# Kernel tuning notes

Measured on AMD Instinct MI355X. Metric: run time of the kernel, lower is better.

The kernel has to match this reference:

```python
import jax, jax.numpy as jnp
import numpy as np

DIM = 192
HEADS = 6
WS = 8                      # window size (Wh = Ww = 8)
N = WS * WS                 # tokens per window = 64
NW = 1024                   # windows per image (256/8)^2
BATCH = 2
B_ = NW * BATCH             # 2048 windows total
TABLE = (2 * WS - 1) ** 2   # 225 relative-position entries


def _relative_position_index():
    coords = np.stack(np.meshgrid(np.arange(WS), np.arange(WS), indexing='ij'))  # (2,WS,WS)
    cf = coords.reshape(2, -1)                       # (2, N)
    rc = (cf[:, :, None] - cf[:, None, :]).transpose(1, 2, 0).astype(np.int64)  # (N,N,2)
    rc[..., 0] += WS - 1
    rc[..., 1] += WS - 1
    rc[..., 0] *= 2 * WS - 1
    return rc.sum(-1)                                # (N, N) in [0, TABLE)


def setup_inputs() -> dict:
    key = jax.random.key(0)
    ks = jax.random.split(key, 16)
    s = 0.02
    inp = {
        'x': jax.random.normal(ks[0], (B_, N, DIM), jnp.float32),
        'y': jax.random.normal(ks[1], (B_, N, DIM), jnp.float32),
        'mask_x': jnp.zeros((NW, N, N), jnp.float32),
        'mask_y': jnp.zeros((NW, N, N), jnp.float32),
        'qkv_w': jax.random.normal(ks[2], (3 * DIM, DIM), jnp.float32) * s,
        'qkv_b': jnp.zeros((3 * DIM,), jnp.float32),
        'kv_w': jax.random.normal(ks[3], (2 * DIM, DIM), jnp.float32) * s,
        'kv_b': jnp.zeros((2 * DIM,), jnp.float32),
        'rpb_x': jax.random.normal(ks[4], (TABLE, HEADS), jnp.float32) * s,
        'rpb_y': jax.random.normal(ks[5], (TABLE, HEADS), jnp.float32) * s,
        'merge1_w': jax.random.normal(ks[6], (DIM, 2 * DIM), jnp.float32) * s,
        'merge1_b': jnp.zeros((DIM,), jnp.float32),
        'merge2_w': jax.random.normal(ks[7], (DIM, DIM), jnp.float32) * s,
        'merge2_b': jnp.zeros((DIM,), jnp.float32),
        'proj_w': jax.random.normal(ks[8], (DIM, DIM), jnp.float32) * s,
        'proj_b': jnp.zeros((DIM,), jnp.float32),
        'rel_idx': jnp.asarray(_relative_position_index(), jnp.int32),
    }
    return inp


def _attend(q, k, v, table, rel_idx, mask):
    # q,k,v: (B_, H, N, hd); table: (TABLE, H); mask: (nW, N, N)
    b_, h, n, hd = q.shape
    bias = table[rel_idx].transpose(2, 0, 1)                 # (H, N, N)
    attn = jnp.einsum('bhnd,bhmd->bhnm', q, k) + bias[None]  # (B_, H, N, N)
    nW = mask.shape[0]
    attn = attn.reshape(b_ // nW, nW, h, n, n) + mask[None, :, None]
    attn = jax.nn.softmax(attn.reshape(b_, h, n, n), axis=-1)
    out = jnp.einsum('bhnm,bhmd->bhnd', attn, v)             # (B_, H, N, hd)
    return out.transpose(0, 2, 1, 3).reshape(b_, n, h * hd)


def reference(x, y, mask_x, mask_y, qkv_w, qkv_b, kv_w, kv_b, rpb_x, rpb_y,
              merge1_w, merge1_b, merge2_w, merge2_b, proj_w, proj_b, rel_idx):
    b_, n, c = x.shape
    hd = c // HEADS
    scale = hd ** (-0.5)
    qkv = (x @ qkv_w.T + qkv_b).reshape(b_, n, 3, HEADS, hd).transpose(2, 0, 3, 1, 4)
    q, k, v = qkv[0] * scale, qkv[1], qkv[2]
    x_self = _attend(q, k, v, rpb_x, rel_idx, mask_x)
    kv = (y @ kv_w.T + kv_b).reshape(b_, n, 2, HEADS, hd).transpose(2, 0, 3, 1, 4)
    x_cross = _attend(q, kv[0], kv[1], rpb_y, rel_idx, mask_y)
    m = jnp.concatenate([x_self, x_cross], axis=-1) @ merge1_w.T + merge1_b
    m = jax.nn.leaky_relu(m, negative_slope=0.2)
    m = m @ merge2_w.T + merge2_b
    return m @ proj_w.T + proj_b
```

## Files before the change

### kernel.cpp

```cpp
#include <hip/hip_runtime.h>

#define DEVINL __device__ __forceinline__

typedef __attribute__((ext_vector_type(8))) short          s16x8;
typedef __attribute__((ext_vector_type(8))) unsigned short u16x8;
typedef __attribute__((ext_vector_type(4))) unsigned short u16x4;
typedef __attribute__((ext_vector_type(4))) float          f32x4;

DEVINL unsigned short f2b(float f) {
    union { float f; unsigned int u; } c; c.f = f;
    return (unsigned short)((c.u + 0x7FFFu + ((c.u >> 16) & 1u)) >> 16);
}
DEVINL f32x4 mfma16(s16x8 a, s16x8 b, f32x4 c) {
    return __builtin_amdgcn_mfma_f32_16x16x32_bf16(a, b, c, 0, 0, 0);
}

#define QKV_ELEMS 110592
#define KV_ELEMS  73728
#define M1_ELEMS  73728
#define M2_ELEMS  36864
#define PW_ELEMS  36864
#define O_QKV 0
#define O_KV  110592
#define O_M1  184320
#define O_M2  258048
#define O_PW  294912
#define WB_ELEMS 331776
#define WB_BYTES (WB_ELEMS * 2)

#define LD_IN  200
#define LD_K   200
#define LD_VT  72
#define LD_P   72
#define LD_CAT 392
#define LD_M   200
#define OFF_R1 0
#define OFF_R2 12800
#define OFF_R3 25600
#define SMEM_ELEMS 39424
#define CATB OFF_R2

#define SCALE 0.17677669529663687f
#define LOG2E 1.4426950408889634f

__global__ __launch_bounds__(256) void cvt_w(
    const float* __restrict__ a, const float* __restrict__ b, const float* __restrict__ c,
    const float* __restrict__ d, const float* __restrict__ e, unsigned short* __restrict__ o)
{
    int i = (blockIdx.x * 256 + threadIdx.x) * 4;
    if (i >= WB_ELEMS) return;
    const float* s; int off;
    if (i < O_KV)      { s = a; off = i - O_QKV; }
    else if (i < O_M1) { s = b; off = i - O_KV; }
    else if (i < O_M2) { s = c; off = i - O_M1; }
    else if (i < O_PW) { s = d; off = i - O_M2; }
    else               { s = e; off = i - O_PW; }
    float4 v = *(const float4*)(s + off);
    u16x4 r;
    r[0] = f2b(v.x); r[1] = f2b(v.y); r[2] = f2b(v.z); r[3] = f2b(v.w);
    *(u16x4*)(o + i) = r;
}

template<bool WB>
DEVINL s16x8 loadB(const unsigned short* wbp, const float* wfp, int off) {
    if constexpr (WB) {
        return *(const s16x8*)(wbp + off);
    } else {
        float4 v0 = *(const float4*)(wfp + off);
        float4 v1 = *(const float4*)(wfp + off + 4);
        s16x8 r;
        r[0] = (short)f2b(v0.x); r[1] = (short)f2b(v0.y); r[2] = (short)f2b(v0.z); r[3] = (short)f2b(v0.w);
        r[4] = (short)f2b(v1.x); r[5] = (short)f2b(v1.y); r[6] = (short)f2b(v1.z); r[7] = (short)f2b(v1.w);
        return r;
    }
}

template<bool WB>
__global__ __launch_bounds__(512, 2) void swin_fused(
    const float* __restrict__ x,
    const float* __restrict__ y,
    const float* __restrict__ mask_x,
    const float* __restrict__ mask_y,
    const float* __restrict__ qkv_w,
    const float* __restrict__ qkv_b,
    const float* __restrict__ kv_w,
    const float* __restrict__ kv_b,
    const float* __restrict__ rpb_x,
    const float* __restrict__ rpb_y,
    const float* __restrict__ m1w,
    const float* __restrict__ m1b,
    const float* __restrict__ m2w,
    const float* __restrict__ m2b,
    const float* __restrict__ pw,
    const float* __restrict__ pb,
    const int* __restrict__ rel_idx,
    const unsigned short* __restrict__ wb,
    float* __restrict__ out)
{
    __shared__ __align__(16) unsigned short smem[SMEM_ELEMS];

    const int tid  = threadIdx.x;
    const int w    = tid >> 6;
    const int lane = tid & 63;
    const int l16  = lane & 15;
    const int quad = lane >> 4;
    const int wm   = w >> 2;
    const int wn   = w & 3;
    const int rb   = w >> 1;
    const int hh   = w & 1;
    const int b    = blockIdx.x;
    const int widx = b & 1023;

    const unsigned short* wqkv = WB ? wb + O_QKV : nullptr;
    const unsigned short* wkv  = WB ? wb + O_KV  : nullptr;
    const unsigned short* wm1  = WB ? wb + O_M1  : nullptr;
    const unsigned short* wm2  = WB ? wb + O_M2  : nullptr;
    const unsigned short* wpw  = WB ? wb + O_PW  : nullptr;

    {
        const float4* gx = (const float4*)(x + (size_t)b * 64 * 192);
        #pragma unroll
        for (int it = 0; it < 3; ++it) {
            int c = it * 512 + tid;
            int e = c * 8;
            int row = e / 192, col = e - row * 192;
            float4 v0 = gx[c * 2], v1 = gx[c * 2 + 1];
            u16x8 r;
            r[0] = f2b(v0.x); r[1] = f2b(v0.y); r[2] = f2b(v0.z); r[3] = f2b(v0.w);
            r[4] = f2b(v1.x); r[5] = f2b(v1.y); r[6] = f2b(v1.z); r[7] = f2b(v1.w);
            *(u16x8*)&smem[OFF_R1 + row * LD_IN + col] = r;
        }
    }
    __syncthreads();

    {
        s16x8 afr[2][6];
        #pragma unroll
        for (int mt = 0; mt < 2; ++mt)
            #pragma unroll
            for (int ks = 0; ks < 6; ++ks)
                afr[mt][ks] = *(const s16x8*)&smem[OFF_R1 + (wm * 32 + mt * 16 + l16) * LD_IN + ks * 32 + quad * 8];
        __syncthreads();

        #pragma unroll
        for (int nt = 0; nt < 9; ++nt) {
            int n0  = wn * 144 + nt * 16;
            int col = n0 + l16;
            f32x4 acc0 = {0,0,0,0}, acc1 = {0,0,0,0};
            #pragma unroll
            for (int ks = 0; ks < 6; ++ks) {
                s16x8 bf = loadB<WB>(wqkv, qkv_w, col * 192 + ks * 32 + quad * 8);
                acc0 = mfma16(afr[0][ks], bf, acc0);
                acc1 = mfma16(afr[1][ks], bf, acc1);
            }
            f32x4 accv[2] = {acc0, acc1};
            float bias = qkv_b[col];
            if (n0 < 192) {
                #pragma unroll
                for (int mt = 0; mt < 2; ++mt)
                    #pragma unroll
                    for (int r = 0; r < 4; ++r)
                        smem[OFF_R1 + (wm * 32 + mt * 16 + quad * 4 + r) * LD_K + col] =
                            f2b((accv[mt][r] + bias) * SCALE);
            } else if (n0 < 384) {
                #pragma unroll
                for (int mt = 0; mt < 2; ++mt)
                    #pragma unroll
                    for (int r = 0; r < 4; ++r)
                        smem[OFF_R2 + (wm * 32 + mt * 16 + quad * 4 + r) * LD_K + (col - 192)] =
                            f2b(accv[mt][r] + bias);
            } else {
                #pragma unroll
                for (int mt = 0; mt < 2; ++mt)
                    #pragma unroll
                    for (int r = 0; r < 4; ++r)
                        smem[OFF_R3 + (col - 384) * LD_VT + (wm * 32 + mt * 16 + quad * 4 + r)] =
                            f2b(accv[mt][r] + bias);
            }
        }
    }
    __syncthreads();

    s16x8 aQ[3];
    #pragma unroll
    for (int hl = 0; hl < 3; ++hl)
        aQ[hl] = *(const s16x8*)&smem[OFF_R1 + (rb * 16 + l16) * LD_K + (hh * 3 + hl) * 32 + quad * 8];
    __syncthreads();

    auto do_attn = [&](const float* __restrict__ rpb,
                       const float* __restrict__ mask,
                       unsigned (&opk)[12]) {
        f32x4 oacc[3][2];
        #pragma unroll
        for (int hl = 0; hl < 3; ++hl) { f32x4 z = {0,0,0,0}; oacc[hl][0] = z; oacc[hl][1] = z; }
        int   idxv[16];
        float maskv[16];
        #pragma unroll
        for (int i = 0; i < 16; ++i) {
            int ntt = i >> 2, r = i & 3;
            int row = rb * 16 + quad * 4 + r;
            int col = ntt * 16 + l16;
            idxv[i]  = rel_idx[row * 64 + col];
            maskv[i] = mask[(size_t)widx * 4096 + row * 64 + col];
        }
        const int pbase = OFF_R1 + w * 16 * LD_P;
        #pragma unroll
        for (int hl = 0; hl < 3; ++hl) {
            int h = hh * 3 + hl;
            f32x4 sacc[4];
            #pragma unroll
            for (int ntt = 0; ntt < 4; ++ntt) {
                s16x8 bK = *(const s16x8*)&smem[OFF_R2 + (ntt * 16 + l16) * LD_K + h * 32 + quad * 8];
                f32x4 z = {0,0,0,0};
                sacc[ntt] = mfma16(aQ[hl], bK, z);
            }
            float sv[4][4];
            #pragma unroll
            for (int ntt = 0; ntt < 4; ++ntt)
                #pragma unroll
                for (int r = 0; r < 4; ++r)
                    sv[ntt][r] = sacc[ntt][r] + rpb[idxv[ntt * 4 + r] * 6 + h] + maskv[ntt * 4 + r];
            float pv[4][4];
            #pragma unroll
            for (int r = 0; r < 4; ++r) {
                float mx = fmaxf(fmaxf(sv[0][r], sv[1][r]), fmaxf(sv[2][r], sv[3][r]));
                mx = fmaxf(mx, __shfl_xor(mx, 1));
                mx = fmaxf(mx, __shfl_xor(mx, 2));
                mx = fmaxf(mx, __shfl_xor(mx, 4));
                mx = fmaxf(mx, __shfl_xor(mx, 8));
                float e0 = __builtin_amdgcn_exp2f((sv[0][r] - mx) * LOG2E);
                float e1 = __builtin_amdgcn_exp2f((sv[1][r] - mx) * LOG2E);
                float e2 = __builtin_amdgcn_exp2f((sv[2][r] - mx) * LOG2E);
                float e3 = __builtin_amdgcn_exp2f((sv[3][r] - mx) * LOG2E);
                float s = e0 + e1 + e2 + e3;
                s += __shfl_xor(s, 1);
                s += __shfl_xor(s, 2);
                s += __shfl_xor(s, 4);
                s += __shfl_xor(s, 8);
                float inv = __builtin_amdgcn_rcpf(s);
                pv[0][r] = e0 * inv; pv[1][r] = e1 * inv; pv[2][r] = e2 * inv; pv[3][r] = e3 * inv;
            }
            #pragma unroll
            for (int ntt = 0; ntt < 4; ++ntt)
                #pragma unroll
                for (int r = 0; r < 4; ++r)
                    smem[pbase + (quad * 4 + r) * LD_P + ntt * 16 + l16] = f2b(pv[ntt][r]);
            #pragma unroll
            for (int nd = 0; nd < 2; ++nd) {
                f32x4 o = oacc[hl][nd];
                #pragma unroll
                for (int kt = 0; kt < 2; ++kt) {
                    s16x8 aP = *(const s16x8*)&smem[pbase + l16 * LD_P + kt * 32 + quad * 8];
                    s16x8 bV = *(const s16x8*)&smem[OFF_R3 + (h * 32 + nd * 16 + l16) * LD_VT + kt * 32 + quad * 8];
                    o = mfma16(aP, bV, o);
                }
                oacc[hl][nd] = o;
            }
        }
        #pragma unroll
        for (int hl = 0; hl < 3; ++hl)
            #pragma unroll
            for (int r = 0; r < 4; ++r)
                opk[hl * 4 + r] = (unsigned)f2b(oacc[hl][0][r]) |
                                  ((unsigned)f2b(oacc[hl][1][r]) << 16);
    };

    unsigned opks[12];
    do_attn(rpb_x, mask_x, opks);
    __syncthreads();

    {
        const float4* gy = (const float4*)(y + (size_t)b * 64 * 192);
        #pragma unroll
        for (int it = 0; it < 3; ++it) {
            int c = it * 512 + tid;
            int e = c * 8;
            int row = e / 192, col = e - row * 192;
            float4 v0 = gy[c * 2], v1 = gy[c * 2 + 1];
            u16x8 r;
            r[0] = f2b(v0.x); r[1] = f2b(v0.y); r[2] = f2b(v0.z); r[3] = f2b(v0.w);
            r[4] = f2b(v1.x); r[5] = f2b(v1.y); r[6] = f2b(v1.z); r[7] = f2b(v1.w);
            *(u16x8*)&smem[OFF_R1 + row * LD_IN + col] = r;
        }
    }
    __syncthreads();

    {
        s16x8 afr[2][6];
        #pragma unroll
        for (int mt = 0; mt < 2; ++mt)
            #pragma unroll
            for (int ks = 0; ks < 6; ++ks)
                afr[mt][ks] = *(const s16x8*)&smem[OFF_R1 + (wm * 32 + mt * 16 + l16) * LD_IN + ks * 32 + quad * 8];

        #pragma unroll
        for (int nt = 0; nt < 6; ++nt) {
            int n0  = wn * 96 + nt * 16;
            int col = n0 + l16;
            f32x4 acc0 = {0,0,0,0}, acc1 = {0,0,0,0};
            #pragma unroll
            for (int ks = 0; ks < 6; ++ks) {
                s16x8 bf = loadB<WB>(wkv, kv_w, col * 192 + ks * 32 + quad * 8);
                acc0 = mfma16(afr[0][ks], bf, acc0);
                acc1 = mfma16(afr[1][ks], bf, acc1);
            }
            f32x4 accv[2] = {acc0, acc1};
            float bias = kv_b[col];
            if (n0 < 192) {
                #pragma unroll
                for (int mt = 0; mt < 2; ++mt)
                    #pragma unroll
                    for (int r = 0; r < 4; ++r)
                        smem[OFF_R2 + (wm * 32 + mt * 16 + quad * 4 + r) * LD_K + col] =
                            f2b(accv[mt][r] + bias);
            } else {
                #pragma unroll
                for (int mt = 0; mt < 2; ++mt)
                    #pragma unroll
                    for (int r = 0; r < 4; ++r)
                        smem[OFF_R3 + (col - 192) * LD_VT + (wm * 32 + mt * 16 + quad * 4 + r)] =
                            f2b(accv[mt][r] + bias);
            }
        }
    }
    __syncthreads();

    unsigned opkc[12];
    do_attn(rpb_y, mask_y, opkc);
    __syncthreads();

    #pragma unroll
    for (int hl = 0; hl < 3; ++hl) {
        int h = hh * 3 + hl;
        #pragma unroll
        for (int r = 0; r < 4; ++r) {
            int row = rb * 16 + quad * 4 + r;
            unsigned ps = opks[hl * 4 + r];
            unsigned pc = opkc[hl * 4 + r];
            smem[CATB + row * LD_CAT + h * 32 + l16]             = (unsigned short)(ps & 0xFFFFu);
            smem[CATB + row * LD_CAT + h * 32 + 16 + l16]        = (unsigned short)(ps >> 16);
            smem[CATB + row * LD_CAT + 192 + h * 32 + l16]       = (unsigned short)(pc & 0xFFFFu);
            smem[CATB + row * LD_CAT + 192 + h * 32 + 16 + l16]  = (unsigned short)(pc >> 16);
        }
    }
    __syncthreads();

    {
        f32x4 acc[3][2];
        #pragma unroll
        for (int nt = 0; nt < 3; ++nt) { f32x4 z = {0,0,0,0}; acc[nt][0] = z; acc[nt][1] = z; }
        #pragma unroll
        for (int ks = 0; ks < 12; ++ks) {
            s16x8 c0 = *(const s16x8*)&smem[CATB + (wm * 32 + l16) * LD_CAT + ks * 32 + quad * 8];
            s16x8 c1 = *(const s16x8*)&smem[CATB + (wm * 32 + 16 + l16) * LD_CAT + ks * 32 + quad * 8];
            #pragma unroll
            for (int nt = 0; nt < 3; ++nt) {
                int col = wn * 48 + nt * 16 + l16;
                s16x8 bf = loadB<WB>(wm1, m1w, col * 384 + ks * 32 + quad * 8);
                acc[nt][0] = mfma16(c0, bf, acc[nt][0]);
                acc[nt][1] = mfma16(c1, bf, acc[nt][1]);
            }
        }
        #pragma unroll
        for (int nt = 0; nt < 3; ++nt) {
            int col = wn * 48 + nt * 16 + l16;
            float bias = m1b[col];
            #pragma unroll
            for (int mt = 0; mt < 2; ++mt)
                #pragma unroll
                for (int r = 0; r < 4; ++r) {
                    float v = acc[nt][mt][r] + bias;
                    v = (v > 0.f) ? v : 0.2f * v;
                    smem[OFF_R1 + (wm * 32 + mt * 16 + quad * 4 + r) * LD_M + col] = f2b(v);
                }
        }
    }
    __syncthreads();

    {
        s16x8 afr[2][6];
        #pragma unroll
        for (int mt = 0; mt < 2; ++mt)
            #pragma unroll
            for (int ks = 0; ks < 6; ++ks)
                afr[mt][ks] = *(const s16x8*)&smem[OFF_R1 + (wm * 32 + mt * 16 + l16) * LD_M + ks * 32 + quad * 8];

        #pragma unroll
        for (int nt = 0; nt < 3; ++nt) {
            int n0  = wn * 48 + nt * 16;
            int col = n0 + l16;
            f32x4 acc0 = {0,0,0,0}, acc1 = {0,0,0,0};
            #pragma unroll
            for (int ks = 0; ks < 6; ++ks) {
                s16x8 bf = loadB<WB>(wm2, m2w, col * 192 + ks * 32 + quad * 8);
                acc0 = mfma16(afr[0][ks], bf, acc0);
                acc1 = mfma16(afr[1][ks], bf, acc1);
            }
            f32x4 accv[2] = {acc0, acc1};
            float bias = m2b[col];
            #pragma unroll
            for (int mt = 0; mt < 2; ++mt)
                #pragma unroll
                for (int r = 0; r < 4; ++r)
                    smem[OFF_R2 + (wm * 32 + mt * 16 + quad * 4 + r) * LD_M + col] = f2b(accv[mt][r] + bias);
        }
    }
    __syncthreads();

    {
        s16x8 afr[2][6];
        #pragma unroll
        for (int mt = 0; mt < 2; ++mt)
            #pragma unroll
            for (int ks = 0; ks < 6; ++ks)
                afr[mt][ks] = *(const s16x8*)&smem[OFF_R2 + (wm * 32 + mt * 16 + l16) * LD_M + ks * 32 + quad * 8];

        #pragma unroll
        for (int nt = 0; nt < 3; ++nt) {
            int n0  = wn * 48 + nt * 16;
            int col = n0 + l16;
            f32x4 acc0 = {0,0,0,0}, acc1 = {0,0,0,0};
            #pragma unroll
            for (int ks = 0; ks < 6; ++ks) {
                s16x8 bf = loadB<WB>(wpw, pw, col * 192 + ks * 32 + quad * 8);
                acc0 = mfma16(afr[0][ks], bf, acc0);
                acc1 = mfma16(afr[1][ks], bf, acc1);
            }
            f32x4 accv[2] = {acc0, acc1};
            float bias = pb[col];
            #pragma unroll
            for (int mt = 0; mt < 2; ++mt)
                #pragma unroll
                for (int r = 0; r < 4; ++r) {
                    int row = wm * 32 + mt * 16 + quad * 4 + r;
                    out[((size_t)b * 64 + row) * 192 + col] = accv[mt][r] + bias;
                }
        }
    }
}

extern "C" void kernel_launch(void* const* d_in, const int* in_sizes, int n_in,
                              void* d_out, int out_size, void* d_ws, size_t ws_size,
                              hipStream_t stream) {
    (void)in_sizes; (void)n_in; (void)out_size;
    const float* x    = (const float*)d_in[0];
    const float* y    = (const float*)d_in[1];
    const float* mx   = (const float*)d_in[2];
    const float* my   = (const float*)d_in[3];
    const float* qw   = (const float*)d_in[4];
    const float* qb   = (const float*)d_in[5];
    const float* kw   = (const float*)d_in[6];
    const float* kb   = (const float*)d_in[7];
    const float* rx   = (const float*)d_in[8];
    const float* ry   = (const float*)d_in[9];
    const float* m1w  = (const float*)d_in[10];
    const float* m1b  = (const float*)d_in[11];
    const float* m2w  = (const float*)d_in[12];
    const float* m2b  = (const float*)d_in[13];
    const float* pw   = (const float*)d_in[14];
    const float* pb   = (const float*)d_in[15];
    const int*   ridx = (const int*)d_in[16];
    float* out = (float*)d_out;

    if (ws_size >= (size_t)WB_BYTES) {
        unsigned short* wbuf = (unsigned short*)d_ws;
        cvt_w<<<WB_ELEMS / 4 / 256, 256, 0, stream>>>(qw, kw, m1w, m2w, pw, wbuf);
        swin_fused<true><<<2048, 512, 0, stream>>>(
            x, y, mx, my, qw, qb, kw, kb, rx, ry, m1w, m1b, m2w, m2b, pw, pb, ridx,
            wbuf, out);
    } else {
        swin_fused<false><<<2048, 512, 0, stream>>>(
            x, y, mx, my, qw, qb, kw, kb, rx, ry, m1w, m1b, m2w, m2b, pw, pb, ridx,
            nullptr, out);
    }
}
```

Before: 652.9 us.

## Raise occupancy to four blocks per SM by trimming attention register usage

Changes launch bounds from 2 to 4 blocks of 512 threads per CU, which caps registers per thread far more tightly. To fit, relative-position indices are pre-multiplied by 6 and packed two per 32-bit register. Mask values are now reloaded from global memory per head instead of held in registers. The output accumulators are also finalized per head rather than kept live across all three heads. The intent is more resident waves to hide latency, at the risk of spills, repeated mask loads, and LDS limits preventing the extra occupancy.

After: 652.3 us. About the same (-0.1%).

```diff
diff --git a/kernel.cpp b/kernel.cpp
--- a/kernel.cpp
+++ b/kernel.cpp
@@ -76,7 +76,7 @@
 }
 
 template<bool WB>
-__global__ __launch_bounds__(512, 2) void swin_fused(
+__global__ __launch_bounds__(512, 4) void swin_fused(
     const float* __restrict__ x,
     const float* __restrict__ y,
     const float* __restrict__ mask_x,
@@ -190,19 +190,17 @@
     auto do_attn = [&](const float* __restrict__ rpb,
                        const float* __restrict__ mask,
                        unsigned (&opk)[12]) {
-        f32x4 oacc[3][2];
-        #pragma unroll
-        for (int hl = 0; hl < 3; ++hl) { f32x4 z = {0,0,0,0}; oacc[hl][0] = z; oacc[hl][1] = z; }
-        int   idxv[16];
-        float maskv[16];
-        #pragma unroll
-        for (int i = 0; i < 16; ++i) {
-            int ntt = i >> 2, r = i & 3;
-            int row = rb * 16 + quad * 4 + r;
+        unsigned idxp[8];
+        #pragma unroll
+        for (int p = 0; p < 8; ++p) {
+            int ntt = p >> 1, r0 = (p & 1) * 2;
+            int row = rb * 16 + quad * 4;
             int col = ntt * 16 + l16;
-            idxv[i]  = rel_idx[row * 64 + col];
-            maskv[i] = mask[(size_t)widx * 4096 + row * 64 + col];
-        }
+            unsigned lo = (unsigned)rel_idx[(row + r0)     * 64 + col] * 6u;
+            unsigned hi = (unsigned)rel_idx[(row + r0 + 1) * 64 + col] * 6u;
+            idxp[p] = lo | (hi << 16);
+        }
+        const float* mrow = mask + (size_t)widx * 4096 + (rb * 16 + quad * 4) * 64 + l16;
         const int pbase = OFF_R1 + w * 16 * LD_P;
         #pragma unroll
         for (int hl = 0; hl < 3; ++hl) {
@@ -218,8 +216,10 @@
             #pragma unroll
             for (int ntt = 0; ntt < 4; ++ntt)
                 #pragma unroll
-                for (int r = 0; r < 4; ++r)
-                    sv[ntt][r] = sacc[ntt][r] + rpb[idxv[ntt * 4 + r] * 6 + h] + maskv[ntt * 4 + r];
+                for (int r = 0; r < 4; ++r) {
+                    unsigned idx6 = (idxp[ntt * 2 + (r >> 1)] >> ((r & 1) * 16)) & 0xFFFFu;
+                    sv[ntt][r] = sacc[ntt][r] + rpb[idx6 + h] + mrow[r * 64 + ntt * 16];
+                }
             float pv[4][4];
             #pragma unroll
             for (int r = 0; r < 4; ++r) {
@@ -245,24 +245,19 @@
                 #pragma unroll
                 for (int r = 0; r < 4; ++r)
                     smem[pbase + (quad * 4 + r) * LD_P + ntt * 16 + l16] = f2b(pv[ntt][r]);
-            #pragma unroll
-            for (int nd = 0; nd < 2; ++nd) {
-                f32x4 o = oacc[hl][nd];
-                #pragma unroll
-                for (int kt = 0; kt < 2; ++kt) {
-                    s16x8 aP = *(const s16x8*)&smem[pbase + l16 * LD_P + kt * 32 + quad * 8];
-                    s16x8 bV = *(const s16x8*)&smem[OFF_R3 + (h * 32 + nd * 16 + l16) * LD_VT + kt * 32 + quad * 8];
-                    o = mfma16(aP, bV, o);
-                }
-                oacc[hl][nd] = o;
-            }
-        }
-        #pragma unroll
-        for (int hl = 0; hl < 3; ++hl)
+            f32x4 oh0 = {0,0,0,0}, oh1 = {0,0,0,0};
+            #pragma unroll
+            for (int kt = 0; kt < 2; ++kt) {
+                s16x8 aP  = *(const s16x8*)&smem[pbase + l16 * LD_P + kt * 32 + quad * 8];
+                s16x8 bV0 = *(const s16x8*)&smem[OFF_R3 + (h * 32 + l16) * LD_VT + kt * 32 + quad * 8];
+                s16x8 bV1 = *(const s16x8*)&smem[OFF_R3 + (h * 32 + 16 + l16) * LD_VT + kt * 32 + quad * 8];
+                oh0 = mfma16(aP, bV0, oh0);
+                oh1 = mfma16(aP, bV1, oh1);
+            }
             #pragma unroll
             for (int r = 0; r < 4; ++r)
-                opk[hl * 4 + r] = (unsigned)f2b(oacc[hl][0][r]) |
-                                  ((unsigned)f2b(oacc[hl][1][r]) << 16);
+                opk[hl * 4 + r] = (unsigned)f2b(oh0[r]) | ((unsigned)f2b(oh1[r]) << 16);
+        }
     };
 
     unsigned opks[12];
```
